# Kernel optimization log

Measured on AMD Instinct MI355X. Metric: run time of the kernel, lower is better.

## Reference

```python
import jax, jax.numpy as jnp
import numpy as np

H, DH, M, DIN = 8, 64, 32, 512  # heads, head_dim, cluster_num, input_dim
INNER = H * DH


def setup_inputs() -> dict:
    key = jax.random.key(0)
    ks = jax.random.split(key, 12)
    s = 0.02
    B, N = 4, 16384
    return {
        "x": jax.random.normal(ks[0], (B, N, DIN), jnp.float32),
        "Wx": jax.random.normal(ks[1], (INNER, DIN), jnp.float32) * s,
        "bx": jnp.zeros((INNER,), jnp.float32),
        "Wfx": jax.random.normal(ks[2], (INNER, DIN), jnp.float32) * s,
        "bfx": jnp.zeros((INNER,), jnp.float32),
        "Wslice": jax.random.normal(ks[3], (M, DH), jnp.float32) * s,
        "bslice": jnp.zeros((M,), jnp.float32),
        "Wq": jax.random.normal(ks[4], (DH, DH), jnp.float32) * s,
        "Wk": jax.random.normal(ks[5], (DH, DH), jnp.float32) * s,
        "Wv": jax.random.normal(ks[6], (DH, DH), jnp.float32) * s,
        "Wout": jax.random.normal(ks[7], (DIN, INNER), jnp.float32) * s,
        "bout": jnp.zeros((DIN,), jnp.float32),
        "temperature": jnp.full((1, H, 1, 1), 0.5, jnp.float32),
    }


def reference(x, Wx, bx, Wfx, bfx, Wslice, bslice, Wq, Wk, Wv, Wout, bout, temperature):
    B, N, D = x.shape
    scale = DH ** -0.5
    # projections -> [B, H, N, DH]
    x_mid = (x @ Wx.T + bx).reshape(B, N, H, DH).transpose(0, 2, 1, 3)
    fx_mid = (x @ Wfx.T + bfx).reshape(B, N, H, DH).transpose(0, 2, 1, 3)
    # soft clustering: [B, H, N, M]
    slice_logits = (x_mid @ Wslice.T + bslice) / temperature
    slice_weights = jax.nn.softmax(slice_logits, axis=-1)
    slice_norm = slice_weights.sum(axis=2)  # [B, H, M]
    slice_token = jnp.einsum('bhnd,bhnm->bhmd', fx_mid, slice_weights)
    slice_token = slice_token / (slice_norm[:, :, :, None] + 1e-5)
    # tiny cluster-level attention (M=32)
    q = slice_token @ Wq.T
    k = slice_token @ Wk.T
    v = slice_token @ Wv.T
    attn = jax.nn.softmax(jnp.einsum('bhmd,bhkd->bhmk', q, k) * scale, axis=-1)
    out_slice = jnp.einsum('bhmk,bhkd->bhmd', attn, v)
    # de-slice back to tokens: [B, H, N, DH] -> [B, N, H*DH]
    out_x = jnp.einsum('bhmd,bhnm->bhnd', out_slice, slice_weights)
    out_x = out_x.transpose(0, 2, 1, 3).reshape(B, N, INNER)
    return out_x @ Wout.T + bout
```

## Files before the change

kernel.cpp:

```cpp
#include <hip/hip_runtime.h>

#define B_ 4
#define N_ 16384
#define DIN_ 512
#define H_ 8
#define DH_ 64
#define M_ 32
#define HM_ 256
#define INNER_ 512

typedef _Float16 fp16_t;
typedef _Float16 h8 __attribute__((ext_vector_type(8)));
typedef _Float16 h4 __attribute__((ext_vector_type(4)));
typedef float f4 __attribute__((ext_vector_type(4)));


__device__ __forceinline__ int swz(int n, int hm) {
  return ((((hm >> 3) ^ ((n >> 3) & 3)) << 3) | (hm & 7));
}

__global__ __launch_bounds__(256) void k0_prep(
    const float* __restrict__ Wx, const float* __restrict__ bx,
    const float* __restrict__ Wslice, const float* __restrict__ bslice,
    const float* __restrict__ temperature,
    fp16_t* __restrict__ Wcb, float* __restrict__ bcomp) {
  __shared__ float ws[M_ * DH_];
  const int h = blockIdx.x;
  const int tid = threadIdx.x;
  for (int i = tid; i < M_ * DH_; i += 256) ws[i] = Wslice[i];
  __syncthreads();
  const float invt = 1.0f / temperature[h];
  for (int m = 0; m < M_; ++m) {
    const int hm = h * M_ + m;
    for (int k = tid; k < DIN_; k += 256) {
      float acc = 0.f;
      #pragma unroll 16
      for (int d = 0; d < DH_; ++d)
        acc += ws[m * DH_ + d] * Wx[(size_t)(h * DH_ + d) * DIN_ + k];
      const int tile = (k >> 5) * 16 + (hm >> 4);
      const int ln = (((k >> 3) & 3) << 4) + (hm & 15);
      Wcb[(size_t)tile * 512 + ln * 8 + (k & 7)] = (fp16_t)(acc * invt);
    }
  }
  if (tid < M_) {
    const int m = tid;
    float acc = bslice[m];
    for (int d = 0; d < DH_; ++d) acc += ws[m * DH_ + d] * bx[h * DH_ + d];
    bcomp[h * M_ + m] = acc * invt;
  }
}

__global__ __launch_bounds__(256) void k1_logits(
    const float* __restrict__ x, const fp16_t* __restrict__ Wcb,
    const float* __restrict__ bcomp, fp16_t* __restrict__ w_blk,
    fp16_t* __restrict__ wt_blk, fp16_t* __restrict__ xt_blk) {
  __shared__ __align__(16) fp16_t smem[16896];
  fp16_t* lt = smem;
  const int tid = threadIdx.x;
  const int lane = tid & 63;
  const int wv = tid >> 6;
  const int n0 = blockIdx.x * 64;
  const int b = blockIdx.y;
  f4 acc[4][4] = {};
  const float* xb = x + ((size_t)b * N_ + n0) * DIN_;
  const int lrow = lane & 15;
  const int kb = (lane >> 4) * 8;
  const int xr = tid >> 3, xq = tid & 7;
  const int xt_rt = wv >> 1;
  const int xt_nt = wv & 1;
  const int xt_k = xt_rt * 16 + (lane & 15);
  const int xt_nb = xt_nt * 32 + (lane >> 4) * 8;
  const fp16_t* wp = Wcb + (size_t)(wv * 4) * 512 + lane * 8;

  f4 xv[2];
  h8 bfv[4];
  #pragma unroll
  for (int i = 0; i < 2; ++i)
    xv[i] = *(const f4*)(xb + (size_t)(xr + i * 32) * DIN_ + xq * 4);
  #pragma unroll
  for (int t = 0; t < 4; ++t)
    bfv[t] = *(const h8*)(wp + (size_t)t * 512);
  #pragma unroll
  for (int i = 0; i < 2; ++i) {
    h4 hv = {(fp16_t)xv[i].x, (fp16_t)xv[i].y, (fp16_t)xv[i].z, (fp16_t)xv[i].w};
    *(h4*)&smem[(xr + i * 32) * 40 + xq * 4] = hv;
  }
  __syncthreads();

  for (int kt = 0; kt < 16; ++kt) {
    fp16_t* lxc = smem + (kt & 1) * 2560;
    fp16_t* lxn = smem + ((kt & 1) ^ 1) * 2560;
    h8 bf[4];
    #pragma unroll
    for (int t = 0; t < 4; ++t) bf[t] = bfv[t];
    if (kt < 15) {
      const int k0n = (kt + 1) * 32;
      #pragma unroll
      for (int i = 0; i < 2; ++i)
        xv[i] = *(const f4*)(xb + (size_t)(xr + i * 32) * DIN_ + k0n + xq * 4);
      #pragma unroll
      for (int t = 0; t < 4; ++t)
        bfv[t] = *(const h8*)(wp + (size_t)((kt + 1) * 16 + t) * 512);
    }
    {
      h8 tx;
      #pragma unroll
      for (int e = 0; e < 8; ++e) tx[e] = lxc[(xt_nb + e) * 40 + xt_k];
      *(h8*)(xt_blk + (((size_t)(b * 32 + kt * 2 + xt_rt) * (N_ / 32)) + (n0 >> 5) + xt_nt) * 512 + lane * 8) = tx;
    }
    h8 af[4];
    #pragma unroll
    for (int t = 0; t < 4; ++t) af[t] = *(const h8*)&lxc[(t * 16 + lrow) * 40 + kb];
    #pragma unroll
    for (int tn = 0; tn < 4; ++tn)
      #pragma unroll
      for (int tc = 0; tc < 4; ++tc)
        acc[tn][tc] = __builtin_amdgcn_mfma_f32_16x16x32_f16(af[tn], bf[tc], acc[tn][tc], 0, 0, 0);
    if (kt < 15) {
      #pragma unroll
      for (int i = 0; i < 2; ++i) {
        h4 hv = {(fp16_t)xv[i].x, (fp16_t)xv[i].y, (fp16_t)xv[i].z, (fp16_t)xv[i].w};
        *(h4*)&lxn[(xr + i * 32) * 40 + xq * 4] = hv;
      }
    }
    __syncthreads();
  }

  const int col = lane & 15;
  const int rgrp = (lane >> 4) * 4;
  float bc[2][2];
  #pragma unroll
  for (int s = 0; s < 2; ++s) {
    bc[s][0] = bcomp[wv * 64 + s * 32 + col];
    bc[s][1] = bcomp[wv * 64 + s * 32 + 16 + col];
  }
  #pragma unroll
  for (int s = 0; s < 2; ++s) {
    const int hmA = wv * 64 + s * 32 + col;
    #pragma unroll
    for (int tn = 0; tn < 4; ++tn)
      #pragma unroll
      for (int r = 0; r < 4; ++r) {
        const int nl = tn * 16 + rgrp + r;
        lt[nl * 264 + swz(nl, hmA)] = (fp16_t)(acc[tn][2 * s][r] + bc[s][0]);
        lt[nl * 264 + swz(nl, hmA + 16)] = (fp16_t)(acc[tn][2 * s + 1][r] + bc[s][1]);
      }
  }
  __syncthreads();

  #pragma unroll
  for (int p = 0; p < 2; ++p) {
    const int pair = tid + p * 256;
    const int nl = pair >> 3, h = pair & 7;
    const int sw = (nl >> 3) & 3;
    h8 ch[4];
    #pragma unroll
    for (int q = 0; q < 4; ++q)
      ch[q] = *(const h8*)&lt[nl * 264 + ((h * 4 + q) ^ sw) * 8];
    float v[32];
    #pragma unroll
    for (int q = 0; q < 4; ++q)
      #pragma unroll
      for (int e = 0; e < 8; ++e) v[q * 8 + e] = (float)ch[q][e];
    float mx = v[0];
    #pragma unroll
    for (int j = 1; j < 32; ++j) mx = fmaxf(mx, v[j]);
    float sm = 0.f;
    #pragma unroll
    for (int j = 0; j < 32; ++j) { v[j] = __expf(v[j] - mx); sm += v[j]; }
    const float inv = __builtin_amdgcn_rcpf(sm);
    h8 oc[4];
    #pragma unroll
    for (int q = 0; q < 4; ++q)
      #pragma unroll
      for (int e = 0; e < 8; ++e) oc[q][e] = (fp16_t)(v[q * 8 + e] * inv);
    #pragma unroll
    for (int q = 0; q < 4; ++q)
      *(h8*)&lt[nl * 264 + ((h * 4 + q) ^ sw) * 8] = oc[q];
  }
  __syncthreads();

  #pragma unroll
  for (int p = 0; p < 8; ++p) {
    const int tile = p * 4 + wv;
    const int nt_l = tile >> 3, hmb = tile & 7;
    const int n_l = nt_l * 16 + (lane & 15);
    const int g = hmb * 4 + (lane >> 4);
    const int sw = (n_l >> 3) & 3;
    h8 v = *(const h8*)&lt[n_l * 264 + (g ^ sw) * 8];
    *(h8*)(w_blk + (((size_t)(b * (N_ / 16) + (n0 >> 4) + nt_l)) * 8 + hmb) * 512 + lane * 8) = v;
  }

  #pragma unroll
  for (int p = 0; p < 8; ++p) {
    const int tile = p * 4 + wv;
    const int hmt = tile >> 1, ntl = tile & 1;
    const int hm = hmt * 16 + (lane & 15);
    const int nb = ntl * 32 + (lane >> 4) * 8;
    h8 v;
    #pragma unroll
    for (int e = 0; e < 8; ++e) {
      const int n = nb + e;
      v[e] = lt[n * 264 + swz(n, hm)];
    }
    *(h8*)(wt_blk + (((size_t)(b * 16 + hmt)) * (N_ / 32) + (n0 >> 5) + ntl) * 512 + lane * 8) = v;
  }
}

__global__ __launch_bounds__(256) void k2_S(
    const fp16_t* __restrict__ wt_blk, const fp16_t* __restrict__ xt_blk,
    float* __restrict__ S, float* __restrict__ norm) {
  const int tid = threadIdx.x, lane = tid & 63, wv = tid >> 6;
  const int hm0 = (blockIdx.x & 1) * 128;
  const int kc0 = (blockIdx.x >> 1) * 128;
  const int nt0 = blockIdx.y * 16;
  const int b = blockIdx.z;
  const int hmw = (wv & 1) * 64, kw = (wv >> 1) * 64;
  const int hmt0 = (hm0 + hmw) >> 4;
  const int kt0 = (kc0 + kw) >> 4;
  const fp16_t* ap = wt_blk + (((size_t)(b * 16 + hmt0)) * (N_ / 32) + nt0) * 512 + lane * 8;
  const fp16_t* bp = xt_blk + (((size_t)(b * 32 + kt0)) * (N_ / 32) + nt0) * 512 + lane * 8;
  const size_t arow = (size_t)(N_ / 32) * 512;
  f4 acc[4][4] = {};
  float ns[4] = {0.f, 0.f, 0.f, 0.f};
  const bool do_norm = (kc0 == 0) && (kw == 0);

  for (int it = 0; it < 16; ++it) {
    h8 af[4], bf[4];
    #pragma unroll
    for (int t = 0; t < 4; ++t) af[t] = *(const h8*)(ap + (size_t)t * arow + it * 512);
    #pragma unroll
    for (int t = 0; t < 4; ++t) bf[t] = *(const h8*)(bp + (size_t)t * arow + it * 512);
    #pragma unroll
    for (int tn = 0; tn < 4; ++tn)
      #pragma unroll
      for (int tc = 0; tc < 4; ++tc)
        acc[tn][tc] = __builtin_amdgcn_mfma_f32_16x16x32_f16(af[tn], bf[tc], acc[tn][tc], 0, 0, 0);
    if (do_norm) {
      #pragma unroll
      for (int t = 0; t < 4; ++t)
        #pragma unroll
        for (int e = 0; e < 8; ++e) ns[t] += (float)af[t][e];
    }
  }

  if (do_norm) {
    #pragma unroll
    for (int t = 0; t < 4; ++t) {
      ns[t] += __shfl_xor(ns[t], 16);
      ns[t] += __shfl_xor(ns[t], 32);
    }
    if (lane < 16) {
      #pragma unroll
      for (int t = 0; t < 4; ++t)
        atomicAdd(&norm[b * HM_ + (hmt0 + t) * 16 + lane], ns[t]);
    }
  }
  const int rg = (lane >> 4) * 4;
  #pragma unroll
  for (int tn = 0; tn < 4; ++tn)
    #pragma unroll
    for (int tc = 0; tc < 4; ++tc)
      #pragma unroll
      for (int r = 0; r < 4; ++r) {
        const int hm = hm0 + hmw + tn * 16 + rg + r;
        const int k = kc0 + kw + tc * 16 + (lane & 15);
        atomicAdd(&S[((size_t)b * HM_ + hm) * DIN_ + k], acc[tn][tc][r]);
      }
}

__global__ __launch_bounds__(256) void k3a_st(
    const float* __restrict__ S, const float* __restrict__ Wfx,
    const float* __restrict__ bfx, const float* __restrict__ norm,
    float* __restrict__ st) {
  const int mq = blockIdx.x;
  const int h = blockIdx.y;
  const int b = blockIdx.z;
  const int tid = threadIdx.x;
  const int m = mq * 4 + (tid >> 6);
  const int d = tid & 63;
  const float* sr = S + ((size_t)b * HM_ + h * M_ + m) * DIN_;
  const float* wr = Wfx + (size_t)(h * DH_ + d) * DIN_;
  float acc = 0.f;
  #pragma unroll 8
  for (int k = 0; k < DIN_; k += 4) {
    f4 a = *(const f4*)(sr + k);
    f4 bb = *(const f4*)(wr + k);
    acc += a.x * bb.x + a.y * bb.y + a.z * bb.z + a.w * bb.w;
  }
  const float nr = norm[b * HM_ + h * M_ + m];
  st[(((size_t)b * H_ + h) * M_ + m) * DH_ + d] =
      (acc + bfx[h * DH_ + d] * nr) / (nr + 1e-5f);
}

__global__ __launch_bounds__(256) void k3b_attn(
    const float* __restrict__ st_g, const float* __restrict__ Wq,
    const float* __restrict__ Wk, const float* __restrict__ Wv,
    float* __restrict__ os_g) {
  __shared__ float st[32][65], qs[32][65], ks[32][65], vs[32][65], at[32][33];
  const int h = blockIdx.x, b = blockIdx.y, tid = threadIdx.x;
  const float* stp = st_g + ((size_t)b * H_ + h) * M_ * DH_;
  for (int i = tid; i < 2048; i += 256) st[i >> 6][i & 63] = stp[i];
  __syncthreads();
  for (int i = tid; i < 2048; i += 256) {
    const int m = i >> 6, d = i & 63;
    float aq = 0, ak = 0, av = 0;
    #pragma unroll 8
    for (int dd = 0; dd < 64; ++dd) {
      const float s = st[m][dd];
      aq += s * Wq[d * 64 + dd];
      ak += s * Wk[d * 64 + dd];
      av += s * Wv[d * 64 + dd];
    }
    qs[m][d] = aq; ks[m][d] = ak; vs[m][d] = av;
  }
  __syncthreads();
  for (int i = tid; i < 1024; i += 256) {
    const int m = i >> 5, j = i & 31;
    float a = 0;
    #pragma unroll 8
    for (int d = 0; d < 64; ++d) a += qs[m][d] * ks[j][d];
    at[m][j] = a * 0.125f;
  }
  __syncthreads();
  if (tid < 32) {
    const int m = tid;
    float mx = -1e30f;
    for (int j = 0; j < 32; ++j) mx = fmaxf(mx, at[m][j]);
    float sm = 0;
    for (int j = 0; j < 32; ++j) { const float e = __expf(at[m][j] - mx); at[m][j] = e; sm += e; }
    const float inv = 1.0f / sm;
    for (int j = 0; j < 32; ++j) at[m][j] *= inv;
  }
  __syncthreads();
  float* osp = os_g + ((size_t)b * H_ + h) * M_ * DH_;
  for (int i = tid; i < 2048; i += 256) {
    const int m = i >> 6, d = i & 63;
    float a = 0;
    #pragma unroll 8
    for (int j = 0; j < 32; ++j) a += at[m][j] * vs[j][d];
    osp[i] = a;
  }
}

__global__ __launch_bounds__(256) void k3c_ct(
    const float* __restrict__ os_g, const float* __restrict__ Wout,
    fp16_t* __restrict__ Ct_blk) {
  const int tid = threadIdx.x, lane = tid & 63, wv = tid >> 6;
  const int b = blockIdx.y;
  const int ti = blockIdx.x * 4 + wv;
  const int kkt = ti >> 3, hmb = ti & 7;
  const int kk = kkt * 16 + (lane & 15);
  h8 outv;
  #pragma unroll
  for (int e = 0; e < 8; ++e) {
    const int hm = hmb * 32 + (lane >> 4) * 8 + e;
    const int h = hm >> 5, m = hm & 31;
    const float* op = os_g + (((size_t)b * H_ + h) * M_ + m) * DH_;
    const float* wp = Wout + (size_t)kk * INNER_ + h * DH_;
    float acc = 0.f;
    #pragma unroll
    for (int d = 0; d < 64; d += 4) {
      f4 a = *(const f4*)(op + d);
      f4 w4 = *(const f4*)(wp + d);
      acc += a.x * w4.x + a.y * w4.y + a.z * w4.z + a.w * w4.w;
    }
    outv[e] = (fp16_t)acc;
  }
  *(h8*)(Ct_blk + (((size_t)(b * 32 + kkt)) * 8 + hmb) * 512 + lane * 8) = outv;
}

__global__ __launch_bounds__(256) void k4_out(
    const fp16_t* __restrict__ w_blk, const fp16_t* __restrict__ Ct_blk,
    const float* __restrict__ bout, float* __restrict__ out) {
  const int tid = threadIdx.x, lane = tid & 63, wv = tid >> 6;
  const int kk0 = blockIdx.x * 128;
  const int n0 = blockIdx.y * 128;
  const int b = blockIdx.z;
  const int nh = (wv & 1) * 64, kh = (wv >> 1) * 64;
  const int nt0 = (n0 + nh) >> 4;
  const int kkt0 = (kk0 + kh) >> 4;
  const fp16_t* ap = w_blk + ((size_t)(b * (N_ / 16) + nt0)) * 8 * 512 + lane * 8;
  const fp16_t* bp = Ct_blk + ((size_t)(b * 32 + kkt0)) * 8 * 512 + lane * 8;
  f4 acc[4][4] = {};

  #pragma unroll
  for (int hmb = 0; hmb < 8; ++hmb) {
    h8 af[4], bf[4];
    #pragma unroll
    for (int t = 0; t < 4; ++t) af[t] = *(const h8*)(ap + (size_t)t * 8 * 512 + hmb * 512);
    #pragma unroll
    for (int t = 0; t < 4; ++t) bf[t] = *(const h8*)(bp + (size_t)t * 8 * 512 + hmb * 512);
    #pragma unroll
    for (int tn = 0; tn < 4; ++tn)
      #pragma unroll
      for (int tc = 0; tc < 4; ++tc)
        acc[tn][tc] = __builtin_amdgcn_mfma_f32_16x16x32_f16(af[tn], bf[tc], acc[tn][tc], 0, 0, 0);
  }
  const int rg = (lane >> 4) * 4;
  #pragma unroll
  for (int tc = 0; tc < 4; ++tc) {
    const int kk = kk0 + kh + tc * 16 + (lane & 15);
    const float bo = bout[kk];
    #pragma unroll
    for (int tn = 0; tn < 4; ++tn)
      #pragma unroll
      for (int r = 0; r < 4; ++r) {
        const int n = n0 + nh + tn * 16 + rg + r;
        out[((size_t)b * N_ + n) * DIN_ + kk] = acc[tn][tc][r] + bo;
      }
  }
}

extern "C" void kernel_launch(void* const* d_in, const int* in_sizes, int n_in,
                              void* d_out, int out_size, void* d_ws, size_t ws_size,
                              hipStream_t stream) {
  (void)in_sizes; (void)n_in; (void)out_size; (void)ws_size;
  const float* x       = (const float*)d_in[0];
  const float* Wx      = (const float*)d_in[1];
  const float* bx      = (const float*)d_in[2];
  const float* Wfx     = (const float*)d_in[3];
  const float* bfx     = (const float*)d_in[4];
  const float* Wslice  = (const float*)d_in[5];
  const float* bslice  = (const float*)d_in[6];
  const float* Wq      = (const float*)d_in[7];
  const float* Wk      = (const float*)d_in[8];
  const float* Wv      = (const float*)d_in[9];
  const float* Wout    = (const float*)d_in[10];
  const float* bout    = (const float*)d_in[11];
  const float* temp    = (const float*)d_in[12];
  float* out = (float*)d_out;

  char* ws = (char*)d_ws;
  fp16_t* w_blk  = (fp16_t*)ws;
  fp16_t* wt_blk = (fp16_t*)(ws + 33554432);
  fp16_t* xt_blk = (fp16_t*)(ws + 67108864);
  float*  S      = (float*)(ws + 134217728);
  float*  norm   = (float*)(ws + 136314880);
  float*  st     = (float*)(ws + 136318976);
  float*  os     = (float*)(ws + 136581120);
  fp16_t* Ct_blk = (fp16_t*)(ws + 136843264);
  fp16_t* Wcb    = (fp16_t*)(ws + 137891840);
  float*  bcomp  = (float*)(ws + 138153984);

  hipMemsetAsync(S, 0, (size_t)B_ * HM_ * DIN_ * 4, stream);
  hipMemsetAsync(norm, 0, (size_t)B_ * HM_ * 4, stream);
  k0_prep<<<dim3(H_), 256, 0, stream>>>(Wx, bx, Wslice, bslice, temp, Wcb, bcomp);
  k1_logits<<<dim3(N_ / 64, B_), 256, 0, stream>>>(x, Wcb, bcomp, w_blk, wt_blk, xt_blk);
  k2_S<<<dim3(8, 32, B_), 256, 0, stream>>>(wt_blk, xt_blk, S, norm);
  k3a_st<<<dim3(8, H_, B_), 256, 0, stream>>>(S, Wfx, bfx, norm, st);
  k3b_attn<<<dim3(H_, B_), 256, 0, stream>>>(st, Wq, Wk, Wv, os);
  k3c_ct<<<dim3(64, B_), 256, 0, stream>>>(os, Wout, Ct_blk);
  k4_out<<<dim3(DIN_ / 128, N_ / 128, B_), 256, 0, stream>>>(w_blk, Ct_blk, bout, out);
}
```

Before: 547.2 us.

## Replace atomic split-K accumulation in S with partial buffers plus reduction kernel

The S reduction kernel now writes per-partition partial sums to a scratch buffer instead of issuing float atomics into S, and a new reduce kernel sums the 16 partitions. Each block handles twice as many N tiles (fewer partitions), and the inner loop is double-buffered so the next tile's fragments load while MFMAs run on the current one. This removes atomic contention and the memset of S, at the cost of an extra 32 MB-class partial buffer write/read and an additional kernel launch, and halves the grid size of k2.

```diff
diff --git a/kernel.cpp b/kernel.cpp
--- a/kernel.cpp
+++ b/kernel.cpp
@@ -8,6 +8,8 @@
 #define M_ 32
 #define HM_ 256
 #define INNER_ 512
+#define K2_PARTS 16
+#define K2_NIT 32
 
 typedef _Float16 fp16_t;
 typedef _Float16 h8 __attribute__((ext_vector_type(8)));
@@ -209,11 +211,12 @@
 
 __global__ __launch_bounds__(256) void k2_S(
     const fp16_t* __restrict__ wt_blk, const fp16_t* __restrict__ xt_blk,
-    float* __restrict__ S, float* __restrict__ norm) {
+    float* __restrict__ P, float* __restrict__ norm) {
   const int tid = threadIdx.x, lane = tid & 63, wv = tid >> 6;
   const int hm0 = (blockIdx.x & 1) * 128;
   const int kc0 = (blockIdx.x >> 1) * 128;
-  const int nt0 = blockIdx.y * 16;
+  const int part = blockIdx.y;
+  const int nt0 = part * K2_NIT;
   const int b = blockIdx.z;
   const int hmw = (wv & 1) * 64, kw = (wv >> 1) * 64;
   const int hmt0 = (hm0 + hmw) >> 4;
@@ -225,22 +228,46 @@
   float ns[4] = {0.f, 0.f, 0.f, 0.f};
   const bool do_norm = (kc0 == 0) && (kw == 0);
 
-  for (int it = 0; it < 16; ++it) {
-    h8 af[4], bf[4];
-    #pragma unroll
-    for (int t = 0; t < 4; ++t) af[t] = *(const h8*)(ap + (size_t)t * arow + it * 512);
-    #pragma unroll
-    for (int t = 0; t < 4; ++t) bf[t] = *(const h8*)(bp + (size_t)t * arow + it * 512);
+  h8 aA[4], bA[4], aB[4], bB[4];
+  #pragma unroll
+  for (int t = 0; t < 4; ++t) {
+    aA[t] = *(const h8*)(ap + (size_t)t * arow);
+    bA[t] = *(const h8*)(bp + (size_t)t * arow);
+  }
+  for (int it = 0; it < K2_NIT; it += 2) {
+    #pragma unroll
+    for (int t = 0; t < 4; ++t) {
+      aB[t] = *(const h8*)(ap + (size_t)t * arow + (it + 1) * 512);
+      bB[t] = *(const h8*)(bp + (size_t)t * arow + (it + 1) * 512);
+    }
     #pragma unroll
     for (int tn = 0; tn < 4; ++tn)
       #pragma unroll
       for (int tc = 0; tc < 4; ++tc)
-        acc[tn][tc] = __builtin_amdgcn_mfma_f32_16x16x32_f16(af[tn], bf[tc], acc[tn][tc], 0, 0, 0);
+        acc[tn][tc] = __builtin_amdgcn_mfma_f32_16x16x32_f16(aA[tn], bA[tc], acc[tn][tc], 0, 0, 0);
     if (do_norm) {
       #pragma unroll
       for (int t = 0; t < 4; ++t)
         #pragma unroll
-        for (int e = 0; e < 8; ++e) ns[t] += (float)af[t][e];
+        for (int e = 0; e < 8; ++e) ns[t] += (float)aA[t][e];
+    }
+    if (it + 2 < K2_NIT) {
+      #pragma unroll
+      for (int t = 0; t < 4; ++t) {
+        aA[t] = *(const h8*)(ap + (size_t)t * arow + (it + 2) * 512);
+        bA[t] = *(const h8*)(bp + (size_t)t * arow + (it + 2) * 512);
+      }
+    }
+    #pragma unroll
+    for (int tn = 0; tn < 4; ++tn)
+      #pragma unroll
+      for (int tc = 0; tc < 4; ++tc)
+        acc[tn][tc] = __builtin_amdgcn_mfma_f32_16x16x32_f16(aB[tn], bB[tc], acc[tn][tc], 0, 0, 0);
+    if (do_norm) {
+      #pragma unroll
+      for (int t = 0; t < 4; ++t)
+        #pragma unroll
+        for (int e = 0; e < 8; ++e) ns[t] += (float)aB[t][e];
     }
   }
 
@@ -256,17 +283,26 @@
         atomicAdd(&norm[b * HM_ + (hmt0 + t) * 16 + lane], ns[t]);
     }
   }
+  float* Pp = P + (((size_t)part * B_ + b) * HM_ + hm0 + hmw) * DIN_ + kc0 + kw;
   const int rg = (lane >> 4) * 4;
   #pragma unroll
   for (int tn = 0; tn < 4; ++tn)
     #pragma unroll
     for (int tc = 0; tc < 4; ++tc)
       #pragma unroll
-      for (int r = 0; r < 4; ++r) {
-        const int hm = hm0 + hmw + tn * 16 + rg + r;
-        const int k = kc0 + kw + tc * 16 + (lane & 15);
-        atomicAdd(&S[((size_t)b * HM_ + hm) * DIN_ + k], acc[tn][tc][r]);
-      }
+      for (int r = 0; r < 4; ++r)
+        Pp[(size_t)(tn * 16 + rg + r) * DIN_ + tc * 16 + (lane & 15)] = acc[tn][tc][r];
+}
+
+__global__ __launch_bounds__(256) void k2r_reduce(
+    const float* __restrict__ P, float* __restrict__ S) {
+  const size_t idx = (size_t)blockIdx.x * 256 + threadIdx.x;
+  const f4* P4 = (const f4*)P;
+  f4 a = P4[idx];
+  #pragma unroll
+  for (int p = 1; p < K2_PARTS; ++p)
+    a += P4[(size_t)p * (B_ * HM_ * DIN_ / 4) + idx];
+  ((f4*)S)[idx] = a;
 }
 
 __global__ __launch_bounds__(256) void k3a_st(
@@ -442,12 +478,13 @@
   fp16_t* Ct_blk = (fp16_t*)(ws + 136843264);
   fp16_t* Wcb    = (fp16_t*)(ws + 137891840);
   float*  bcomp  = (float*)(ws + 138153984);
-
-  hipMemsetAsync(S, 0, (size_t)B_ * HM_ * DIN_ * 4, stream);
+  float*  P      = (float*)(ws + 138158080);
+
   hipMemsetAsync(norm, 0, (size_t)B_ * HM_ * 4, stream);
   k0_prep<<<dim3(H_), 256, 0, stream>>>(Wx, bx, Wslice, bslice, temp, Wcb, bcomp);
   k1_logits<<<dim3(N_ / 64, B_), 256, 0, stream>>>(x, Wcb, bcomp, w_blk, wt_blk, xt_blk);
-  k2_S<<<dim3(8, 32, B_), 256, 0, stream>>>(wt_blk, xt_blk, S, norm);
+  k2_S<<<dim3(8, K2_PARTS, B_), 256, 0, stream>>>(wt_blk, xt_blk, P, norm);
+  k2r_reduce<<<dim3(B_ * HM_ * DIN_ / 4 / 256), 256, 0, stream>>>(P, S);
   k3a_st<<<dim3(8, H_, B_), 256, 0, stream>>>(S, Wfx, bfx, norm, st);
   k3b_attn<<<dim3(H_, B_), 256, 0, stream>>>(st, Wq, Wk, Wv, os);
   k3c_ct<<<dim3(64, B_), 256, 0, stream>>>(os, Wout, Ct_blk);
```

Result: faster. 525.9 us (-3.9%).
